# Performance work log

Measured on AMD Instinct MI355X. Metric: run time of the kernel, lower is better.

## Reference

```python
import jax, jax.numpy as jnp
import numpy as np

HIDDEN = 2048
NUM_HEADS = 16
HEAD_DIM = HIDDEN // NUM_HEADS


def setup_inputs() -> dict:
    key = jax.random.key(0)
    ks = jax.random.split(key, 5)
    B, S, H = 2, 2048, HIDDEN
    # xavier_uniform bounds
    qkv_bound = float(np.sqrt(6.0 / (H + 3 * H)))
    out_bound = float(np.sqrt(6.0 / (H + H)))
    return {
        "x": jax.random.normal(ks[0], (B, S, H), dtype=jnp.float32),
        "W_qkv": jax.random.uniform(ks[1], (3 * H, H), minval=-qkv_bound, maxval=qkv_bound, dtype=jnp.float32),
        "b_qkv": jnp.zeros((3 * H,), dtype=jnp.float32),
        "W_out": jax.random.uniform(ks[2], (H, H), minval=-out_bound, maxval=out_bound, dtype=jnp.float32),
        "b_out": jnp.zeros((H,), dtype=jnp.float32),
    }


def reference(x, W_qkv, b_qkv, W_out, b_out):
    B, S, H = x.shape
    # fused QKV projection (torch Linear: x @ W.T + b)
    qkv = x @ W_qkv.T + b_qkv                      # (B, S, 3H)
    q, k, v = jnp.split(qkv, 3, axis=-1)
    # (B, S, H) -> (B, N, S, D)
    def to_heads(t):
        return t.reshape(B, S, NUM_HEADS, HEAD_DIM).transpose(0, 2, 1, 3)
    q, k, v = to_heads(q), to_heads(k), to_heads(v)
    scale = HEAD_DIM ** -0.5
    scores = jnp.einsum("bnqd,bnkd->bnqk", q, k) * scale  # (B, N, S, S)
    causal = jnp.triu(jnp.ones((S, S), dtype=bool), k=1)
    scores = jnp.where(causal, -jnp.inf, scores)
    attn = jax.nn.softmax(scores, axis=-1)
    out = jnp.einsum("bnqk,bnkd->bnqd", attn, v)           # (B, N, S, D)
    out = out.transpose(0, 2, 1, 3).reshape(B, S, H)
    return out @ W_out.T + b_out
```

## Files before the change

### kernel.cpp

```cpp
#include <hip/hip_runtime.h>
#include <stdint.h>


using bf16x8 = __attribute__((ext_vector_type(8))) __bf16;
using f32x4  = __attribute__((ext_vector_type(4))) float;

#define S_LEN 2048
#define HID   2048
#define NHEAD 16
#define DHEAD 128
#define QSCALE_L2E (0.08838834764831845f * 1.4426950408889634f)

__device__ __forceinline__ unsigned short f2bf(float f) {
  union { float f; unsigned int u; } c; c.f = f;
  unsigned int u = c.u;
  return (unsigned short)((u + 0x7FFFu + ((u >> 16) & 1u)) >> 16);
}

__device__ __forceinline__ unsigned int pkbf(float a, float b) {
  union { __bf16 h[2]; unsigned int u; } x;
  x.h[0] = (__bf16)a; x.h[1] = (__bf16)b;
  return x.u;
}

__device__ __forceinline__ void gload_lds16(const void* g, void* l) {
  __builtin_amdgcn_global_load_lds(
      (const __attribute__((address_space(1))) unsigned int*)g,
      (__attribute__((address_space(3))) unsigned int*)l, 16, 0, 0);
}

__device__ __forceinline__ f32x4 mfma16(bf16x8 a, bf16x8 b, f32x4 c) {
  return __builtin_amdgcn_mfma_f32_16x16x32_bf16(a, b, c, 0, 0, 0);
}

__device__ __forceinline__ float hmax4(f32x4 v) {
  return fmaxf(fmaxf(v[0], v[1]), fmaxf(v[2], v[3]));
}

__global__ void cvt_bf16(const float* __restrict__ in, unsigned short* __restrict__ out, int n) {
  const int n4 = n >> 2;
  const int stride = gridDim.x * blockDim.x;
  for (int i = blockIdx.x * blockDim.x + threadIdx.x; i < n4; i += stride) {
    float4 v = reinterpret_cast<const float4*>(in)[i];
    ushort4 o;
    o.x = f2bf(v.x); o.y = f2bf(v.y); o.z = f2bf(v.z); o.w = f2bf(v.w);
    reinterpret_cast<ushort4*>(out)[i] = o;
  }
}

template<int EPI>
__global__ __launch_bounds__(256) void gemm_bt(
    const unsigned short* __restrict__ A, const unsigned short* __restrict__ Bw,
    const float* __restrict__ bias, int K, int N,
    unsigned short* __restrict__ q_out, unsigned short* __restrict__ k_out,
    unsigned short* __restrict__ vt_out, float* __restrict__ c_out)
{
  __shared__ char lsA[128 * 128];
  __shared__ char lsB[128 * 128];
  const int tid = threadIdx.x;
  const int l = tid & 63, w = tid >> 6;
  const int wr = w >> 1, wc = w & 1;
  const int bm = blockIdx.x * 128, bn = blockIdx.y * 128;
  const int row16 = l & 15, kg = l >> 4;

  f32x4 acc[4][4] = {};

  for (int k0 = 0; k0 < K; k0 += 64) {
    #pragma unroll
    for (int c = 0; c < 4; ++c) {
      const int o = c * 4096 + tid * 16;
      const int r = o >> 7;
      const int cb = (o & 127) ^ ((r & 7) << 4);
      gload_lds16((const char*)A + ((size_t)(bm + r) * K + k0) * 2 + cb,
                  lsA + c * 4096 + (w << 10));
      gload_lds16((const char*)Bw + ((size_t)(bn + r) * K + k0) * 2 + cb,
                  lsB + c * 4096 + (w << 10));
    }
    __syncthreads();

    #pragma unroll
    for (int h = 0; h < 2; ++h) {
      bf16x8 af[4], bfr[4];
      #pragma unroll
      for (int i = 0; i < 4; ++i) {
        const int ra = wr * 64 + i * 16 + row16;
        af[i]  = *(const bf16x8*)(lsA + ra * 128 + ((h * 64 + kg * 16) ^ ((ra & 7) << 4)));
        const int rb = wc * 64 + i * 16 + row16;
        bfr[i] = *(const bf16x8*)(lsB + rb * 128 + ((h * 64 + kg * 16) ^ ((rb & 7) << 4)));
      }
      #pragma unroll
      for (int i = 0; i < 4; ++i)
        #pragma unroll
        for (int j = 0; j < 4; ++j)
          acc[i][j] = mfma16(af[i], bfr[j], acc[i][j]);
    }
    __syncthreads();
  }

  const int r0 = kg * 4;
  #pragma unroll
  for (int i = 0; i < 4; ++i) {
    const int row = bm + wr * 64 + i * 16 + r0;
    #pragma unroll
    for (int j = 0; j < 4; ++j) {
      const int col = bn + wc * 64 + j * 16 + row16;
      const float bv = bias[col];
      if (EPI == 1) {
        #pragma unroll
        for (int r = 0; r < 4; ++r)
          c_out[(size_t)(row + r) * N + col] = acc[i][j][r] + bv;
      } else {
        const int sec = col >> 11;
        const int within = col & 2047;
        const int head = within >> 7, d = within & 127;
        #pragma unroll
        for (int r = 0; r < 4; ++r) {
          const int rr = row + r;
          const int b = rr >> 11, s = rr & 2047;
          const int bh = b * NHEAD + head;
          const float v = acc[i][j][r] + bv;
          if (sec == 0)
            q_out[((size_t)bh * S_LEN + s) * DHEAD + d] = f2bf(v * QSCALE_L2E);
          else if (sec == 1)
            k_out[((size_t)bh * S_LEN + s) * DHEAD + d] = f2bf(v);
          else
            vt_out[((size_t)bh * DHEAD + d) * S_LEN + s] = f2bf(v);
        }
      }
    }
  }
}

__global__ __launch_bounds__(256, 2) void attn_fwd(
    const unsigned short* __restrict__ Q, const unsigned short* __restrict__ Kk,
    const unsigned short* __restrict__ Vt, unsigned short* __restrict__ O,
    const float* __restrict__ Wout, unsigned short* __restrict__ Woutb)
{
  __shared__ char lsK[2][64 * 256];
  __shared__ char lsV[2][128 * 128];
  __shared__ char lsP[4][32 * 128];
  const int tid = threadIdx.x, l = tid & 63, w = tid >> 6;
  const int row16 = l & 15, kg = l >> 4;
  const int qb = (blockIdx.y < 16) ? (15 - (int)blockIdx.x) : (int)blockIdx.x;
  const int bh = blockIdx.y;
  const int bidx = bh >> 4, head = bh & 15;

  const char* Qh = (const char*)(Q  + (size_t)bh * S_LEN * DHEAD);
  const char* Kh = (const char*)(Kk + (size_t)bh * S_LEN * DHEAD);
  const char* Vh = (const char*)(Vt + (size_t)bh * DHEAD * S_LEN);

  const int q0w = qb * 128 + w * 32;

  bf16x8 qf[2][4];
  #pragma unroll
  for (int qs = 0; qs < 2; ++qs)
    #pragma unroll
    for (int t = 0; t < 4; ++t)
      qf[qs][t] = *(const bf16x8*)(Qh + ((size_t)(q0w + qs * 16 + row16) * DHEAD + t * 32 + kg * 8) * 2);

  float m[2]  = {-1e30f, -1e30f};
  float ls[2] = {0.f, 0.f};
  f32x4 oacc[2][8] = {};

  const int last = 2 * qb + 1;

#define STAGE(buf, kt_) do {                                                     \
    _Pragma("unroll")                                                            \
    for (int c = 0; c < 4; ++c) {                                                \
      const int o = c * 4096 + tid * 16;                                         \
      const int rk = o >> 8, cbk = (o & 255) ^ ((rk & 7) << 4);                  \
      gload_lds16(Kh + (size_t)((kt_) * 64 + rk) * 256 + cbk,                    \
                  lsK[buf] + c * 4096 + (w << 10));                              \
      const int dv = o >> 7, cbv = (o & 127) ^ ((dv & 7) << 4);                  \
      gload_lds16(Vh + (size_t)dv * 4096 + (size_t)(kt_) * 128 + cbv,            \
                  lsV[buf] + c * 4096 + (w << 10));                              \
    } } while (0)

  STAGE(0, 0);

  {
    const int slice = (int)blockIdx.y * 16 + (int)blockIdx.x;
    const float4* src = (const float4*)Wout;
    ushort4* dst = (ushort4*)Woutb;
    const int base = slice * 2048;
    #pragma unroll
    for (int i = 0; i < 8; ++i) {
      float4 v = src[base + i * 256 + tid];
      ushort4 o;
      o.x = f2bf(v.x); o.y = f2bf(v.y); o.z = f2bf(v.z); o.w = f2bf(v.w);
      dst[base + i * 256 + tid] = o;
    }
  }

  __syncthreads();

  int cur = 0;
  for (int kt = 0; ; ++kt) {
    if (kt < last) STAGE(cur ^ 1, kt + 1);

    if (kt * 64 <= q0w + 31) {
      const char* Kc = lsK[cur];
      const char* Vc = lsV[cur];
      char* Pl = lsP[w];

      f32x4 sc[4][2] = {};
      #pragma unroll
      for (int j = 0; j < 4; ++j) {
        const int krow = j * 16 + row16;
        const int sw = (krow & 7) << 4;
        bf16x8 kf[4];
        #pragma unroll
        for (int t = 0; t < 4; ++t)
          kf[t] = *(const bf16x8*)(Kc + krow * 256 + ((t * 64 + kg * 16) ^ sw));
        #pragma unroll
        for (int t = 0; t < 4; ++t) {
          sc[j][0] = mfma16(kf[t], qf[0][t], sc[j][0]);
          sc[j][1] = mfma16(kf[t], qf[1][t], sc[j][1]);
        }
      }

      if (kt >= 2 * qb) {
        #pragma unroll
        for (int j = 0; j < 4; ++j) {
          const int kvb = kt * 64 + j * 16 + kg * 4;
          #pragma unroll
          for (int qs = 0; qs < 2; ++qs) {
            const int qq = q0w + qs * 16 + row16;
            #pragma unroll
            for (int r = 0; r < 4; ++r)
              if (kvb + r > qq) sc[j][qs][r] = -1e30f;
          }
        }
      }

      float pm[2], al[2] = {1.f, 1.f};
      #pragma unroll
      for (int qs = 0; qs < 2; ++qs) {
        float mx = fmaxf(fmaxf(hmax4(sc[0][qs]), hmax4(sc[1][qs])),
                         fmaxf(hmax4(sc[2][qs]), hmax4(sc[3][qs])));
        mx = fmaxf(mx, __shfl_xor(mx, 16, 64));
        mx = fmaxf(mx, __shfl_xor(mx, 32, 64));
        pm[qs] = mx;
      }
      const bool need = (pm[0] > m[0] + 8.f) || (pm[1] > m[1] + 8.f);
      if (__any(need)) {
        const float n0 = fmaxf(m[0], pm[0]), n1 = fmaxf(m[1], pm[1]);
        al[0] = exp2f(m[0] - n0); al[1] = exp2f(m[1] - n1);
        m[0] = n0; m[1] = n1;
        float aq[2][4];
        #pragma unroll
        for (int qs2 = 0; qs2 < 2; ++qs2)
          #pragma unroll
          for (int r = 0; r < 4; ++r)
            aq[qs2][r] = __shfl(al[qs2], kg * 4 + r, 64);
        #pragma unroll
        for (int qs2 = 0; qs2 < 2; ++qs2)
          #pragma unroll
          for (int dt = 0; dt < 8; ++dt)
            #pragma unroll
            for (int r = 0; r < 4; ++r)
              oacc[qs2][dt][r] *= aq[qs2][r];
      }

      #pragma unroll
      for (int qs = 0; qs < 2; ++qs) {
        const int q = qs * 16 + row16;
        const int psw = (q & 7) << 4;
        float ps = 0.f;
        #pragma unroll
        for (int j = 0; j < 4; ++j) {
          const float p0 = exp2f(sc[j][qs][0] - m[qs]);
          const float p1 = exp2f(sc[j][qs][1] - m[qs]);
          const float p2 = exp2f(sc[j][qs][2] - m[qs]);
          const float p3 = exp2f(sc[j][qs][3] - m[qs]);
          ps += (p0 + p1) + (p2 + p3);
          uint2 pw; pw.x = pkbf(p0, p1); pw.y = pkbf(p2, p3);
          *(uint2*)(Pl + q * 128 + ((j * 32 + kg * 8) ^ psw)) = pw;
        }
        ps += __shfl_xor(ps, 16, 64);
        ps += __shfl_xor(ps, 32, 64);
        ls[qs] = ls[qs] * al[qs] + ps;
      }

      bf16x8 pa[2][2];
      #pragma unroll
      for (int qs2 = 0; qs2 < 2; ++qs2) {
        const int q = qs2 * 16 + row16;
        #pragma unroll
        for (int ks = 0; ks < 2; ++ks)
          pa[qs2][ks] = *(const bf16x8*)(Pl + q * 128 + ((ks * 64 + kg * 16) ^ ((q & 7) << 4)));
      }
      #pragma unroll
      for (int dt = 0; dt < 8; ++dt) {
        const int drow = dt * 16 + row16;
        const int vsw = (drow & 7) << 4;
        bf16x8 v0 = *(const bf16x8*)(Vc + drow * 128 + ((kg * 16) ^ vsw));
        bf16x8 v1 = *(const bf16x8*)(Vc + drow * 128 + ((64 + kg * 16) ^ vsw));
        oacc[0][dt] = mfma16(pa[0][0], v0, oacc[0][dt]);
        oacc[0][dt] = mfma16(pa[0][1], v1, oacc[0][dt]);
        oacc[1][dt] = mfma16(pa[1][0], v0, oacc[1][dt]);
        oacc[1][dt] = mfma16(pa[1][1], v1, oacc[1][dt]);
      }
    }

    __syncthreads();
    if (kt == last) break;
    cur ^= 1;
  }
#undef STAGE

  #pragma unroll
  for (int qs2 = 0; qs2 < 2; ++qs2) {
    #pragma unroll
    for (int r = 0; r < 4; ++r) {
      const float lr = __shfl(ls[qs2], kg * 4 + r, 64);
      const float inv = 1.0f / lr;
      const int q = q0w + qs2 * 16 + kg * 4 + r;
      const size_t orow = (size_t)(bidx * S_LEN + q) * HID + (size_t)head * DHEAD;
      #pragma unroll
      for (int dt = 0; dt < 8; ++dt)
        O[orow + dt * 16 + row16] = f2bf(oacc[qs2][dt][r] * inv);
    }
  }
}

extern "C" void kernel_launch(void* const* d_in, const int* in_sizes, int n_in,
                              void* d_out, int out_size, void* d_ws, size_t ws_size,
                              hipStream_t stream) {
  const float* x    = (const float*)d_in[0];
  const float* Wqkv = (const float*)d_in[1];
  const float* bqkv = (const float*)d_in[2];
  const float* Wout = (const float*)d_in[3];
  const float* bout = (const float*)d_in[4];
  float* out = (float*)d_out;

  if (ws_size < 100663296) return;
  char* ws = (char*)d_ws;
  unsigned short* Qb    = (unsigned short*)(ws);
  unsigned short* Kb    = (unsigned short*)(ws + 16777216);
  unsigned short* Vtb   = (unsigned short*)(ws + 2 * 16777216);
  unsigned short* xb    = (unsigned short*)(ws + 3 * 16777216);
  unsigned short* Ob    = xb;
  unsigned short* Wqkvb = (unsigned short*)(ws + 4 * 16777216);
  unsigned short* Woutb = (unsigned short*)(ws + 4 * 16777216 + 25165824);

  cvt_bf16<<<2048, 256, 0, stream>>>(x,    xb,    4096 * 2048);
  cvt_bf16<<<2048, 256, 0, stream>>>(Wqkv, Wqkvb, 6144 * 2048);

  gemm_bt<0><<<dim3(32, 48), 256, 0, stream>>>(xb, Wqkvb, bqkv, 2048, 6144,
                                               Qb, Kb, Vtb, nullptr);
  attn_fwd<<<dim3(16, 32), 256, 0, stream>>>(Qb, Kb, Vtb, Ob, Wout, Woutb);
  gemm_bt<1><<<dim3(32, 16), 256, 0, stream>>>(Ob, Woutb, bout, 2048, 2048,
                                               nullptr, nullptr, nullptr, out);
}
```

Before: 282.9 us.

## Stage GEMM epilogues through LDS for coalesced 16-byte stores and merge conversions

Both GEMM epilogues now write their accumulator tiles into a swizzled shared-memory buffer (the reused A/B staging area) and then write them out with coalesced 16-byte global stores. In the QKV case this also handles the V transpose inside LDS, replacing the old scattered 2-byte stores. The two fp32-to-bf16 conversion launches are merged into a single kernel to remove one launch. In exchange the epilogue gains extra LDS traffic and one or two barriers.

```diff
diff --git a/kernel.cpp b/kernel.cpp
--- a/kernel.cpp
+++ b/kernel.cpp
@@ -37,14 +37,18 @@
   return fmaxf(fmaxf(v[0], v[1]), fmaxf(v[2], v[3]));
 }
 
-__global__ void cvt_bf16(const float* __restrict__ in, unsigned short* __restrict__ out, int n) {
-  const int n4 = n >> 2;
+__global__ void cvt_two(const float* __restrict__ a, unsigned short* __restrict__ ao, int na4,
+                        const float* __restrict__ b, unsigned short* __restrict__ bo, int nb4) {
   const int stride = gridDim.x * blockDim.x;
-  for (int i = blockIdx.x * blockDim.x + threadIdx.x; i < n4; i += stride) {
-    float4 v = reinterpret_cast<const float4*>(in)[i];
+  const int tot = na4 + nb4;
+  for (int i = blockIdx.x * blockDim.x + threadIdx.x; i < tot; i += stride) {
+    const float4* src; ushort4* dst; int idx;
+    if (i < na4) { src = (const float4*)a; dst = (ushort4*)ao; idx = i; }
+    else         { src = (const float4*)b; dst = (ushort4*)bo; idx = i - na4; }
+    float4 v = src[idx];
     ushort4 o;
     o.x = f2bf(v.x); o.y = f2bf(v.y); o.z = f2bf(v.z); o.w = f2bf(v.w);
-    reinterpret_cast<ushort4*>(out)[i] = o;
+    dst[idx] = o;
   }
 }
 
@@ -55,8 +59,9 @@
     unsigned short* __restrict__ q_out, unsigned short* __restrict__ k_out,
     unsigned short* __restrict__ vt_out, float* __restrict__ c_out)
 {
-  __shared__ char lsA[128 * 128];
-  __shared__ char lsB[128 * 128];
+  __shared__ __align__(16) char lds[32768];
+  char* lsA = lds;
+  char* lsB = lds + 16384;
   const int tid = threadIdx.x;
   const int l = tid & 63, w = tid >> 6;
   const int wr = w >> 1, wc = w & 1;
@@ -97,35 +102,89 @@
     __syncthreads();
   }
 
-  const int r0 = kg * 4;
-  #pragma unroll
-  for (int i = 0; i < 4; ++i) {
-    const int row = bm + wr * 64 + i * 16 + r0;
-    #pragma unroll
-    for (int j = 0; j < 4; ++j) {
-      const int col = bn + wc * 64 + j * 16 + row16;
-      const float bv = bias[col];
-      if (EPI == 1) {
-        #pragma unroll
-        for (int r = 0; r < 4; ++r)
-          c_out[(size_t)(row + r) * N + col] = acc[i][j][r] + bv;
-      } else {
-        const int sec = col >> 11;
-        const int within = col & 2047;
-        const int head = within >> 7, d = within & 127;
-        #pragma unroll
-        for (int r = 0; r < 4; ++r) {
-          const int rr = row + r;
-          const int b = rr >> 11, s = rr & 2047;
-          const int bh = b * NHEAD + head;
-          const float v = acc[i][j][r] + bv;
-          if (sec == 0)
-            q_out[((size_t)bh * S_LEN + s) * DHEAD + d] = f2bf(v * QSCALE_L2E);
-          else if (sec == 1)
-            k_out[((size_t)bh * S_LEN + s) * DHEAD + d] = f2bf(v);
-          else
-            vt_out[((size_t)bh * DHEAD + d) * S_LEN + s] = f2bf(v);
-        }
+  if (EPI == 1) {
+    #pragma unroll
+    for (int p = 0; p < 2; ++p) {
+      if (wr == p) {
+        #pragma unroll
+        for (int i = 0; i < 4; ++i) {
+          #pragma unroll
+          for (int j = 0; j < 4; ++j) {
+            const int c = wc * 64 + j * 16 + row16;
+            const float bv = bias[bn + c];
+            #pragma unroll
+            for (int r = 0; r < 4; ++r) {
+              const int Rl = i * 16 + kg * 4 + r;
+              *(float*)(lds + Rl * 512 + ((c * 4) ^ ((Rl & 7) << 4))) = acc[i][j][r] + bv;
+            }
+          }
+        }
+      }
+      __syncthreads();
+      #pragma unroll
+      for (int it = 0; it < 8; ++it) {
+        const int o = it * 4096 + tid * 16;
+        const int rw = o >> 9, cb = o & 511;
+        uint4 v = *(const uint4*)(lds + rw * 512 + (cb ^ ((rw & 7) << 4)));
+        *(uint4*)((char*)c_out + ((size_t)(bm + p * 64 + rw) * N + bn) * 4 + cb) = v;
+      }
+      __syncthreads();
+    }
+  } else {
+    const int secb  = bn >> 11;
+    const int headb = (bn & 2047) >> 7;
+    const int s0    = bm & 2047;
+    const int bh    = (bm >> 11) * NHEAD + headb;
+
+    if (secb < 2) {
+      #pragma unroll
+      for (int i = 0; i < 4; ++i) {
+        const int R0 = wr * 64 + i * 16 + kg * 4;
+        #pragma unroll
+        for (int j = 0; j < 4; ++j) {
+          const int c = wc * 64 + j * 16 + row16;
+          const float bv = bias[bn + c];
+          #pragma unroll
+          for (int r = 0; r < 4; ++r) {
+            float v = acc[i][j][r] + bv;
+            if (secb == 0) v *= QSCALE_L2E;
+            const int Rr = R0 + r;
+            *(unsigned short*)(lds + Rr * 256 + ((c * 2) ^ ((Rr & 7) << 4))) = f2bf(v);
+          }
+        }
+      }
+      __syncthreads();
+      unsigned short* qk = (secb == 0) ? q_out : k_out;
+      char* gbase = (char*)(qk + ((size_t)bh * S_LEN + s0) * DHEAD);
+      #pragma unroll
+      for (int it = 0; it < 8; ++it) {
+        const int o = it * 4096 + tid * 16;
+        const int s = o >> 8, db = o & 255;
+        uint4 v = *(const uint4*)(lds + s * 256 + (db ^ ((s & 7) << 4)));
+        *(uint4*)(gbase + (size_t)s * 256 + db) = v;
+      }
+    } else {
+      #pragma unroll
+      for (int i = 0; i < 4; ++i) {
+        const int R0 = wr * 64 + i * 16 + kg * 4;
+        #pragma unroll
+        for (int j = 0; j < 4; ++j) {
+          const int c = wc * 64 + j * 16 + row16;
+          const float bv = bias[bn + c];
+          uint2 pw;
+          pw.x = pkbf(acc[i][j][0] + bv, acc[i][j][1] + bv);
+          pw.y = pkbf(acc[i][j][2] + bv, acc[i][j][3] + bv);
+          *(uint2*)(lds + c * 256 + ((R0 * 2) ^ ((c & 7) << 4))) = pw;
+        }
+      }
+      __syncthreads();
+      char* gbase = (char*)vt_out + ((size_t)bh * DHEAD) * (S_LEN * 2) + (size_t)s0 * 2;
+      #pragma unroll
+      for (int it = 0; it < 8; ++it) {
+        const int o = it * 4096 + tid * 16;
+        const int d = o >> 8, sb = o & 255;
+        uint4 v = *(const uint4*)(lds + d * 256 + (sb ^ ((d & 7) << 4)));
+        *(uint4*)(gbase + (size_t)d * (S_LEN * 2) + sb) = v;
       }
     }
   }
@@ -344,8 +403,8 @@
   unsigned short* Wqkvb = (unsigned short*)(ws + 4 * 16777216);
   unsigned short* Woutb = (unsigned short*)(ws + 4 * 16777216 + 25165824);
 
-  cvt_bf16<<<2048, 256, 0, stream>>>(x,    xb,    4096 * 2048);
-  cvt_bf16<<<2048, 256, 0, stream>>>(Wqkv, Wqkvb, 6144 * 2048);
+  cvt_two<<<2048, 256, 0, stream>>>(x, xb, 4096 * 2048 / 4,
+                                    Wqkv, Wqkvb, 6144 * 2048 / 4);
 
   gemm_bt<0><<<dim3(32, 48), 256, 0, stream>>>(xb, Wqkvb, bqkv, 2048, 6144,
                                                Qb, Kb, Vtb, nullptr);
```

Result: faster. 264.4 us (-6.6%).
